# Kernel optimization log

Hardware: AMD Instinct MI355X
Metric: run time of the kernel (lower is better)

Reference implementation:

```python
import jax, jax.numpy as jnp
import numpy as np

B, T, F = 32, 512, 4096
H = 128            # num_lstm
NUM_CLASSES = 2    # dense outputs = NUM_CLASSES + 1 (CTC blank)


def setup_inputs() -> dict:
    key = jax.random.key(0)
    ks = jax.random.split(key, 6)
    x = jax.random.normal(ks[0], (B, T, F), dtype=jnp.float32)
    # Keras LSTM params: kernel [F, 4H], recurrent_kernel [H, 4H], bias [4H]
    # (gate order i, f, c, o). Glorot-ish scaling for stability.
    Wk = jax.random.normal(ks[1], (F, 4 * H), dtype=jnp.float32) / np.sqrt(F)
    Wr = jax.random.normal(ks[2], (H, 4 * H), dtype=jnp.float32) / np.sqrt(H)
    b = jnp.zeros((4 * H,), dtype=jnp.float32).at[H:2 * H].set(1.0)  # unit_forget_bias
    Wd = jax.random.normal(ks[3], (H, NUM_CLASSES + 1), dtype=jnp.float32) / np.sqrt(H)
    bd = jnp.zeros((NUM_CLASSES + 1,), dtype=jnp.float32)
    return {"x": x, "Wk": Wk, "Wr": Wr, "b": b, "Wd": Wd, "bd": bd}


def _lstm(x, Wk, Wr, b):
    # Precompute input projections for all timesteps (big GEMM once).
    z = jnp.einsum("btf,fg->btg", x, Wk) + b          # [B, T, 4H]
    z = jnp.transpose(z, (1, 0, 2))                    # [T, B, 4H]

    def step(carry, z_t):
        h, c = carry
        g = z_t + h @ Wr                               # [B, 4H]
        i = jax.nn.sigmoid(g[:, 0 * H:1 * H])
        f = jax.nn.sigmoid(g[:, 1 * H:2 * H])
        cc = jnp.tanh(g[:, 2 * H:3 * H])
        o = jax.nn.sigmoid(g[:, 3 * H:4 * H])
        c = f * c + i * cc
        h = o * jnp.tanh(c)
        return (h, c), h

    h0 = jnp.zeros((x.shape[0], H), dtype=x.dtype)
    c0 = jnp.zeros((x.shape[0], H), dtype=x.dtype)
    _, hs = jax.lax.scan(step, (h0, c0), z)            # hs: [T, B, H]
    return jnp.transpose(hs, (1, 0, 2))                # [B, T, H]


def reference(x, Wk, Wr, b, Wd, bd):
    # Inference-mode forward (dropout/recurrent_dropout inactive).
    h = _lstm(x, Wk, Wr, b)                            # [B, T, H]
    return h @ Wd + bd                                 # [B, T, num_classes+1]
```

## Files before the change

kernel.cpp:

```cpp
#include <hip/hip_runtime.h>
#include <hip/hip_bf16.h>
#include <hip/hip_fp16.h>
#include <math.h>

#define B_  32
#define T_  512
#define F_  4096
#define H_  128
#define G4H 512
#define NCLS 3
#define M_  (B_ * T_)
#define KSTEPS 128

typedef _Float16 f16x8 __attribute__((ext_vector_type(8)));
typedef _Float16 f16x4 __attribute__((ext_vector_type(4)));
typedef float    f32x4 __attribute__((ext_vector_type(4)));

__device__ __forceinline__ void gl_lds16(const _Float16* g, _Float16* l) {
    __builtin_amdgcn_global_load_lds(
        (const __attribute__((address_space(1))) void*)(g),
        (__attribute__((address_space(3))) void*)(l), 16, 0, 0);
}

__global__ __launch_bounds__(256) void cvt_wkT(
    const float* __restrict__ Wk, _Float16* __restrict__ btK)
{
    __shared__ float ls[64][65];
    const int k0 = blockIdx.x * 64;
    const int n0 = blockIdx.y * 64;
    const int tid = threadIdx.x;

    {
        int r  = tid >> 4;
        int c4 = (tid & 15) * 4;
        #pragma unroll
        for (int p = 0; p < 4; ++p) {
            float4 v = *reinterpret_cast<const float4*>(
                &Wk[(size_t)(k0 + r + p * 16) * G4H + n0 + c4]);
            ls[r + p * 16][c4 + 0] = v.x;
            ls[r + p * 16][c4 + 1] = v.y;
            ls[r + p * 16][c4 + 2] = v.z;
            ls[r + p * 16][c4 + 3] = v.w;
        }
    }
    __syncthreads();
    {
        int rn = tid >> 2;
        int ck = (tid & 3) * 16;
        f16x8 h0, h1;
        #pragma unroll
        for (int j = 0; j < 8; ++j) {
            h0[j] = (_Float16)ls[ck + j][rn];
            h1[j] = (_Float16)ls[ck + 8 + j][rn];
        }
        const int n    = n0 + rn;
        const int kg   = k0 + ck;
        const int kblk = kg >> 5;
        const int kk   = kg & 31;
        const int g0   = kk >> 3;
        const int sw   = (n >> 1) & 3;
        _Float16* base = btK + (size_t)kblk * (512 * 32) + (size_t)n * 32;
        *reinterpret_cast<f16x8*>(base + ((g0 ^ sw) << 3))       = h0;
        *reinterpret_cast<f16x8*>(base + (((g0 + 1) ^ sw) << 3)) = h1;
    }
}

__global__ __launch_bounds__(256) void cvt_wrT(
    const float* __restrict__ Wr, _Float16* __restrict__ wrT)
{
    __shared__ float ls[64][65];
    const int k0 = blockIdx.x * 64;
    const int n0 = blockIdx.y * 64;
    const int tid = threadIdx.x;
    {
        int r  = tid >> 4;
        int c4 = (tid & 15) * 4;
        #pragma unroll
        for (int p = 0; p < 4; ++p) {
            float4 v = *reinterpret_cast<const float4*>(
                &Wr[(size_t)(k0 + r + p * 16) * G4H + n0 + c4]);
            ls[r + p * 16][c4 + 0] = v.x;
            ls[r + p * 16][c4 + 1] = v.y;
            ls[r + p * 16][c4 + 2] = v.z;
            ls[r + p * 16][c4 + 3] = v.w;
        }
    }
    __syncthreads();
    {
        int rn = tid >> 2;
        int ck = (tid & 3) * 16;
        f16x8 h0, h1;
        #pragma unroll
        for (int j = 0; j < 8; ++j) {
            h0[j] = (_Float16)ls[ck + j][rn];
            h1[j] = (_Float16)ls[ck + 8 + j][rn];
        }
        _Float16* dst = &wrT[(size_t)(n0 + rn) * H_ + k0 + ck];
        *reinterpret_cast<f16x8*>(dst)     = h0;
        *reinterpret_cast<f16x8*>(dst + 8) = h1;
    }
}

__device__ __forceinline__ void lds_barrier() {
    asm volatile("s_waitcnt lgkmcnt(0)" ::: "memory");
    __builtin_amdgcn_s_barrier();
    asm volatile("" ::: "memory");
}

__global__ __launch_bounds__(512, 4) void gemm_fused(
    const float* __restrict__ x, const _Float16* __restrict__ btK,
    const float* __restrict__ bias, float* __restrict__ z)
{
    __shared__ __align__(16) _Float16 As[3][64 * 32];
    __shared__ __align__(16) _Float16 Bs[3][256 * 32];

    const int tid = threadIdx.x;
    const int w   = tid >> 6;
    const int l   = tid & 63;
    const int fr  = l & 15;
    const int q   = l >> 4;

    const int bid   = blockIdx.x;
    const int xcd   = bid & 7;
    const int idx   = bid >> 3;
    const int mt    = xcd * 32 + (idx >> 1);
    const int ntile = idx & 1;
    const int m0    = mt * 64;
    const int n0    = ntile * 256;

    const int ar = tid >> 3;
    const int hc = (tid & 7) * 4;
    const int abyte = ((((hc >> 3) ^ ((ar >> 1) & 3)) << 4) | ((hc << 1) & 15));
    const float* xrow = x + (size_t)(m0 + ar) * F_ + hc;

    #define ISSUE_B(t, buf)                                                   \
    {                                                                         \
        const _Float16* ck_ = btK + (size_t)(t) * (512 * 32) + n0 * 32;       \
        gl_lds16(ck_ + w * 1024 + l * 8,       &Bs[buf][w * 1024]);           \
        gl_lds16(ck_ + w * 1024 + 512 + l * 8, &Bs[buf][w * 1024 + 512]);     \
    }

    #define LOADX(t) (*reinterpret_cast<const float4*>(xrow + (size_t)(t) * 32))

    #define WRITE_A(v, buf)                                                   \
    {                                                                         \
        f16x4 hh; hh[0] = (_Float16)v.x; hh[1] = (_Float16)v.y;               \
        hh[2] = (_Float16)v.z; hh[3] = (_Float16)v.w;                         \
        *reinterpret_cast<f16x4*>(                                            \
            reinterpret_cast<char*>(&As[buf][0]) + ar * 64 + abyte) = hh;     \
    }

    #define COMPUTE(buf)                                                      \
    {                                                                         \
        f16x8 af[4], bf[2];                                                   \
        _Pragma("unroll")                                                     \
        for (int i = 0; i < 4; ++i) {                                         \
            int r   = i * 16 + fr;                                            \
            int off = r * 64 + ((q ^ ((r >> 1) & 3)) << 4);                   \
            af[i] = *reinterpret_cast<const f16x8*>(                          \
                reinterpret_cast<const char*>(&As[buf][0]) + off);            \
        }                                                                     \
        _Pragma("unroll")                                                     \
        for (int j = 0; j < 2; ++j) {                                         \
            int n   = w * 32 + j * 16 + fr;                                   \
            int off = n * 64 + ((q ^ ((n >> 1) & 3)) << 4);                   \
            bf[j] = *reinterpret_cast<const f16x8*>(                          \
                reinterpret_cast<const char*>(&Bs[buf][0]) + off);            \
        }                                                                     \
        _Pragma("unroll")                                                     \
        for (int i = 0; i < 4; ++i)                                           \
            _Pragma("unroll")                                                 \
            for (int j = 0; j < 2; ++j)                                       \
                acc[i][j] = __builtin_amdgcn_mfma_f32_16x16x32_f16(           \
                    af[i], bf[j], acc[i][j], 0, 0, 0);                        \
    }

    f32x4 acc[4][2] = {};
    float4 xvA, xvB;

    ISSUE_B(0, 0) xvA = LOADX(0);
    ISSUE_B(1, 1) xvB = LOADX(1);
    WRITE_A(xvA, 0)
    lds_barrier();

    int b0 = 0, b1 = 1, b2 = 2;
    for (int t = 0; t < KSTEPS; t += 2) {
        if (t + 2 < KSTEPS) { ISSUE_B(t + 2, b2) xvA = LOADX(t + 2); }
        if (t + 1 < KSTEPS) WRITE_A(xvB, b1)
        COMPUTE(b0)
        lds_barrier();
        if (t + 3 < KSTEPS) { ISSUE_B(t + 3, b0) xvB = LOADX(t + 3); }
        if (t + 2 < KSTEPS) WRITE_A(xvA, b2)
        COMPUTE(b1)
        lds_barrier();
        int tmp = b2; b2 = b1; b1 = b0; b0 = tmp;
    }
    #undef ISSUE_B
    #undef LOADX
    #undef WRITE_A
    #undef COMPUTE

    #pragma unroll
    for (int j = 0; j < 2; ++j) {
        const int nn = n0 + w * 32 + j * 16 + fr;
        const int ch = (nn & 127) * 4 + (nn >> 7);
        const float bj = bias[nn];
        #pragma unroll
        for (int i = 0; i < 4; ++i)
            #pragma unroll
            for (int r = 0; r < 4; ++r)
                z[(size_t)(m0 + i * 16 + q * 4 + r) * G4H + ch]
                    = acc[i][j][r] + bj;
    }
}

__device__ __forceinline__ float sig_f(float x) {
    return __builtin_amdgcn_rcpf(
        1.0f + __builtin_amdgcn_exp2f(-1.442695040888963f * x));
}
__device__ __forceinline__ float tanh_f(float x) {
    return 1.0f - 2.0f * __builtin_amdgcn_rcpf(
        1.0f + __builtin_amdgcn_exp2f(2.885390081777927f * x));
}

__global__ __launch_bounds__(512, 2) void lstm_mfma(
    const float* __restrict__ z,
    const _Float16* __restrict__ wrT,
    float* __restrict__ hs)
{
    const int b    = blockIdx.x;
    const int tid  = threadIdx.x;
    const int w    = tid >> 6;
    const int lane = tid & 63;
    const int l15  = lane & 15;
    const int q    = lane >> 4;
    const int jj   = w * 16 + l15;

    __shared__ __align__(16) _Float16 hA[2][128];

    f16x8 bf[4][4];
    #pragma unroll
    for (int g = 0; g < 4; ++g)
        #pragma unroll
        for (int kf = 0; kf < 4; ++kf)
            bf[g][kf] = *reinterpret_cast<const f16x8*>(
                &wrT[(size_t)(g * H_ + jj) * H_ + kf * 32 + q * 8]);

    float cstate = 0.f;
    if (tid < 128) reinterpret_cast<unsigned int*>(hA)[tid] = 0u;

    const float* zrow  = z  + (size_t)b * T_ * G4H + jj * 4;
    float*       hbase = hs + (size_t)b * T_ * H_;

    const f32x4 zero4 = {0.f, 0.f, 0.f, 0.f};

    float4 zP0 = *reinterpret_cast<const float4*>(zrow + (size_t)(0 << 9));
    float4 zP1 = *reinterpret_cast<const float4*>(zrow + (size_t)(1 << 9));
    float4 zP2 = *reinterpret_cast<const float4*>(zrow + (size_t)(2 << 9));
    float4 zP3 = *reinterpret_cast<const float4*>(zrow + (size_t)(3 << 9));

    __syncthreads();

    #define LSTM_STEP(t, CUR, ZZ)                                             \
    {                                                                         \
        f16x8 af0 = *reinterpret_cast<const f16x8*>(&hA[CUR][0 * 32 + q * 8]);\
        f16x8 af1 = *reinterpret_cast<const f16x8*>(&hA[CUR][1 * 32 + q * 8]);\
        f16x8 af2 = *reinterpret_cast<const f16x8*>(&hA[CUR][2 * 32 + q * 8]);\
        f16x8 af3 = *reinterpret_cast<const f16x8*>(&hA[CUR][3 * 32 + q * 8]);\
        float zt0_ = ZZ.x, zt1_ = ZZ.y, zt2_ = ZZ.z, zt3_ = ZZ.w;             \
        ZZ = *reinterpret_cast<const float4*>(                                \
            zrow + (size_t)((((t) + 4) & (T_ - 1)) << 9));                    \
        float gv[4];                                                          \
        _Pragma("unroll")                                                     \
        for (int g = 0; g < 4; ++g) {                                         \
            f32x4 aA = __builtin_amdgcn_mfma_f32_16x16x32_f16(                \
                af0, bf[g][0], zero4, 0, 0, 0);                               \
            aA = __builtin_amdgcn_mfma_f32_16x16x32_f16(                      \
                af1, bf[g][1], aA, 0, 0, 0);                                  \
            f32x4 aB = __builtin_amdgcn_mfma_f32_16x16x32_f16(                \
                af2, bf[g][2], zero4, 0, 0, 0);                               \
            aB = __builtin_amdgcn_mfma_f32_16x16x32_f16(                      \
                af3, bf[g][3], aB, 0, 0, 0);                                  \
            gv[g] = aA[0] + aB[0];                                           \
        }                                                                     \
        float iv = sig_f(gv[0] + zt0_);                                       \
        float fv = sig_f(gv[1] + zt1_);                                       \
        float cc = tanh_f(gv[2] + zt2_);                                      \
        float ov = sig_f(gv[3] + zt3_);                                       \
        cstate = fv * cstate + iv * cc;                                       \
        float h = ov * tanh_f(cstate);                                        \
        if (q == 0) {                                                         \
            hA[CUR ^ 1][jj] = (_Float16)h;                                    \
            hbase[((t) << 7) + jj] = h;                                       \
        }                                                                     \
        lds_barrier();                                                        \
    }

    for (int t = 0; t < T_; t += 4) {
        LSTM_STEP(t,     0, zP0)
        LSTM_STEP(t + 1, 1, zP1)
        LSTM_STEP(t + 2, 0, zP2)
        LSTM_STEP(t + 3, 1, zP3)
    }
    #undef LSTM_STEP
}

__global__ __launch_bounds__(256) void dense_out(
    const float* __restrict__ hs, const float* __restrict__ Wd,
    const float* __restrict__ bd, float* __restrict__ out)
{
    int idx = blockIdx.x * 256 + threadIdx.x;
    if (idx >= B_ * T_ * NCLS) return;
    int cls = idx % NCLS;
    int row = idx / NCLS;
    const float* h = hs + (size_t)row * H_;
    float acc = bd[cls];
    #pragma unroll 8
    for (int k = 0; k < H_; ++k) acc += h[k] * Wd[k * NCLS + cls];
    out[idx] = acc;
}

extern "C" void kernel_launch(void* const* d_in, const int* in_sizes, int n_in,
                              void* d_out, int out_size, void* d_ws, size_t ws_size,
                              hipStream_t stream)
{
    const float* x  = (const float*)d_in[0];
    const float* Wk = (const float*)d_in[1];
    const float* Wr = (const float*)d_in[2];
    const float* b  = (const float*)d_in[3];
    const float* Wd = (const float*)d_in[4];
    const float* bd = (const float*)d_in[5];
    float* out = (float*)d_out;

    float*     z   = (float*)d_ws;
    float*     hs  = z + (size_t)M_ * G4H;
    _Float16*  btK = (_Float16*)(hs + (size_t)M_ * H_);
    _Float16*  wrT = btK + (size_t)G4H * F_;

    cvt_wkT<<<dim3(F_ / 64, G4H / 64), 256, 0, stream>>>(Wk, btK);
    cvt_wrT<<<dim3(H_ / 64, G4H / 64), 256, 0, stream>>>(Wr, wrT);
    gemm_fused<<<512, 512, 0, stream>>>(x, btK, b, z);
    lstm_mfma<<<B_, 512, 0, stream>>>(z, wrT, hs);
    int total = B_ * T_ * NCLS;
    dense_out<<<(total + 255) / 256, 256, 0, stream>>>(hs, Wd, bd, out);
}
```

Baseline: 368.9 us.

## Store z in natural gate layout and split LSTM scan into two launches

The GEMM epilogue now writes z in its natural [i|f|c|o] column order rather than an interleaved per-unit layout, so the store pattern is contiguous. The LSTM kernel now reads the four gates as scalar loads strided by 128 floats, where it previously used one float4 load. The recurrence is also split into two kernel launches of 256 steps each, with the cell state and the fp16 hidden state carried through workspace buffers. This probably aims to shorten a single long kernel or to set up later overlap, but it adds a launch, a state handoff through memory, and four loads per step instead of one.

```diff
diff --git a/kernel.cpp b/kernel.cpp
--- a/kernel.cpp
+++ b/kernel.cpp
@@ -203,13 +203,12 @@
     #pragma unroll
     for (int j = 0; j < 2; ++j) {
         const int nn = n0 + w * 32 + j * 16 + fr;
-        const int ch = (nn & 127) * 4 + (nn >> 7);
         const float bj = bias[nn];
         #pragma unroll
         for (int i = 0; i < 4; ++i)
             #pragma unroll
             for (int r = 0; r < 4; ++r)
-                z[(size_t)(m0 + i * 16 + q * 4 + r) * G4H + ch]
+                z[(size_t)(m0 + i * 16 + q * 4 + r) * G4H + nn]
                     = acc[i][j][r] + bj;
     }
 }
@@ -226,7 +225,10 @@
 __global__ __launch_bounds__(512, 2) void lstm_mfma(
     const float* __restrict__ z,
     const _Float16* __restrict__ wrT,
-    float* __restrict__ hs)
+    float* __restrict__ hs,
+    float* __restrict__ cst,
+    _Float16* __restrict__ h16,
+    int t0)
 {
     const int b    = blockIdx.x;
     const int tid  = threadIdx.x;
@@ -246,18 +248,32 @@
             bf[g][kf] = *reinterpret_cast<const f16x8*>(
                 &wrT[(size_t)(g * H_ + jj) * H_ + kf * 32 + q * 8]);
 
-    float cstate = 0.f;
-    if (tid < 128) reinterpret_cast<unsigned int*>(hA)[tid] = 0u;
-
-    const float* zrow  = z  + (size_t)b * T_ * G4H + jj * 4;
+    float cstate;
+    if (t0 == 0) {
+        if (tid < 128) reinterpret_cast<unsigned int*>(hA)[tid] = 0u;
+        cstate = 0.f;
+    } else {
+        if (tid < 64)
+            reinterpret_cast<unsigned int*>(hA[0])[tid] =
+                reinterpret_cast<const unsigned int*>(h16 + (size_t)b * H_)[tid];
+        cstate = cst[(size_t)b * H_ + jj];
+    }
+
+    const float* zq    = z  + (size_t)b * T_ * G4H + jj;
     float*       hbase = hs + (size_t)b * T_ * H_;
 
     const f32x4 zero4 = {0.f, 0.f, 0.f, 0.f};
 
-    float4 zP0 = *reinterpret_cast<const float4*>(zrow + (size_t)(0 << 9));
-    float4 zP1 = *reinterpret_cast<const float4*>(zrow + (size_t)(1 << 9));
-    float4 zP2 = *reinterpret_cast<const float4*>(zrow + (size_t)(2 << 9));
-    float4 zP3 = *reinterpret_cast<const float4*>(zrow + (size_t)(3 << 9));
+    #define LOADZ(t, d)                                                       \
+    {                                                                         \
+        int zo = (((t) & (T_ - 1)) << 9);                                     \
+        d.x = zq[zo];       d.y = zq[zo + 128];                               \
+        d.z = zq[zo + 256]; d.w = zq[zo + 384];                               \
+    }
+
+    float4 zP0, zP1, zP2, zP3;
+    LOADZ(t0 + 0, zP0) LOADZ(t0 + 1, zP1)
+    LOADZ(t0 + 2, zP2) LOADZ(t0 + 3, zP3)
 
     __syncthreads();
 
@@ -268,8 +284,7 @@
         f16x8 af2 = *reinterpret_cast<const f16x8*>(&hA[CUR][2 * 32 + q * 8]);\
         f16x8 af3 = *reinterpret_cast<const f16x8*>(&hA[CUR][3 * 32 + q * 8]);\
         float zt0_ = ZZ.x, zt1_ = ZZ.y, zt2_ = ZZ.z, zt3_ = ZZ.w;             \
-        ZZ = *reinterpret_cast<const float4*>(                                \
-            zrow + (size_t)((((t) + 4) & (T_ - 1)) << 9));                    \
+        LOADZ((t) + 4, ZZ)                                                    \
         float gv[4];                                                          \
         _Pragma("unroll")                                                     \
         for (int g = 0; g < 4; ++g) {                                         \
@@ -281,7 +296,7 @@
                 af2, bf[g][2], zero4, 0, 0, 0);                               \
             aB = __builtin_amdgcn_mfma_f32_16x16x32_f16(                      \
                 af3, bf[g][3], aB, 0, 0, 0);                                  \
-            gv[g] = aA[0] + aB[0];                                           \
+            gv[g] = aA[0] + aB[0];                                            \
         }                                                                     \
         float iv = sig_f(gv[0] + zt0_);                                       \
         float fv = sig_f(gv[1] + zt1_);                                       \
@@ -296,13 +311,19 @@
         lds_barrier();                                                        \
     }
 
-    for (int t = 0; t < T_; t += 4) {
+    for (int t = t0; t < t0 + 256; t += 4) {
         LSTM_STEP(t,     0, zP0)
         LSTM_STEP(t + 1, 1, zP1)
         LSTM_STEP(t + 2, 0, zP2)
         LSTM_STEP(t + 3, 1, zP3)
     }
     #undef LSTM_STEP
+    #undef LOADZ
+
+    if (q == 0) cst[(size_t)b * H_ + jj] = cstate;
+    if (tid < 64)
+        reinterpret_cast<unsigned int*>(h16 + (size_t)b * H_)[tid] =
+            reinterpret_cast<unsigned int*>(hA[0])[tid];
 }
 
 __global__ __launch_bounds__(256) void dense_out(
@@ -336,11 +357,14 @@
     float*     hs  = z + (size_t)M_ * G4H;
     _Float16*  btK = (_Float16*)(hs + (size_t)M_ * H_);
     _Float16*  wrT = btK + (size_t)G4H * F_;
+    float*     cst = (float*)(wrT + (size_t)G4H * H_);
+    _Float16*  h16 = (_Float16*)(cst + (size_t)B_ * H_);
 
     cvt_wkT<<<dim3(F_ / 64, G4H / 64), 256, 0, stream>>>(Wk, btK);
     cvt_wrT<<<dim3(H_ / 64, G4H / 64), 256, 0, stream>>>(Wr, wrT);
     gemm_fused<<<512, 512, 0, stream>>>(x, btK, b, z);
-    lstm_mfma<<<B_, 512, 0, stream>>>(z, wrT, hs);
+    lstm_mfma<<<B_, 512, 0, stream>>>(z, wrT, hs, cst, h16, 0);
+    lstm_mfma<<<B_, 512, 0, stream>>>(z, wrT, hs, cst, h16, 256);
     int total = B_ * T_ * NCLS;
     dense_out<<<(total + 255) / 256, 256, 0, stream>>>(hs, Wd, bd, out);
 }
```

Result: slower. 381.7 us (+3.5%).
